# Kernel optimization log

Measured on AMD Instinct MI355X. Metric: run time of the kernel, lower is better.

## Reference

```python
import jax, jax.numpy as jnp
import numpy as np
from jax import lax

# PointPWC multi-scale Chamfer/Smoothness/Curvature loss (single scale here).
F_CHAMFER = 1.0
F_SMOOTH = 0.5
F_CURVATURE = 0.3
ALPHA0 = 0.02


def _sqdist(src, dst):
    # src: (B,N,3), dst: (B,M,3) -> (B,N,M) squared euclidean distances
    d = -2.0 * jnp.einsum('bnc,bmc->bnm', src, dst)
    d = d + jnp.sum(src * src, axis=-1)[:, :, None]
    d = d + jnp.sum(dst * dst, axis=-1)[:, None, :]
    return d


def _knn(sqd, k):
    # smallest-k of sqd along last axis -> (dists, indices)
    neg, idx = lax.top_k(-sqd, k)
    return -neg, idx


def _group(points, idx):
    # points: (B,N,C), idx: (B,M,k) -> (B,M,k,C)
    return jax.vmap(lambda p, i: p[i])(points, idx)


def _curvature(pc):
    # pc: (B,N,3) -> (B,N,3)
    _, kidx = _knn(_sqdist(pc, pc), 10)
    grouped = _group(pc, kidx)
    return jnp.sum(grouped - pc[:, :, None, :], axis=2) / 9.0


def _curvature_warp(pc, warped):
    _, kidx = _knn(_sqdist(pc, pc), 10)
    grouped = _group(warped, kidx)
    return jnp.sum(grouped - warped[:, :, None, :], axis=2) / 9.0


def _chamfer(p1, p2):
    sqd = _sqdist(p1, p2)
    return jnp.min(sqd, axis=-1), jnp.min(sqd, axis=1)


def _smooth(pc, flow, k):
    _, kidx = _knn(_sqdist(pc, pc), k)
    g = _group(flow, kidx)
    d = g - flow[:, :, None, :]
    sq = jnp.sum(d * d, axis=3)
    # safe norm: zero (self-neighbor) entries get norm 0 with zero grad
    nrm = jnp.where(sq == 0, 0.0, jnp.sqrt(jnp.where(sq == 0, 1.0, sq)))
    return jnp.sum(nrm, axis=2) / 8.0


def _interp_curvature(p1, p2, c2):
    dist, kidx = _knn(_sqdist(p1, p2), 5)
    g = _group(c2, kidx)  # (B,N,5,3)
    w = 1.0 / (dist + 1e-8)
    w = w / jnp.sum(w, axis=2, keepdims=True)
    return jnp.sum(w[..., None] * g, axis=2)


def setup_inputs() -> dict:
    key = jax.random.key(0)
    k1, k2, k3 = jax.random.split(key, 3)
    N = 8192
    coords = jax.random.normal(k1, (N, 3), dtype=jnp.float32)
    registration_gt = jax.random.normal(k2, (1, N, 3), dtype=jnp.float32)
    registration_pred = jax.random.normal(k3, (1, N, 3), dtype=jnp.float32)
    return {
        'registration_pred': registration_pred,
        'registration_gt': registration_gt,
        'coords': coords,
        'smoothness_k': 9,
    }


def reference(registration_pred, registration_gt, coords, smoothness_k):
    pc1 = coords[None]                       # (1,N,3)
    pc2 = coords[None] + registration_gt     # (1,N,3)
    flow = registration_pred                 # (1,N,3)

    pc2_curv = _curvature(pc2)
    pc1_warp = pc1 + flow
    dist1, dist2 = _chamfer(pc1_warp, pc2)
    moved_curv = _curvature_warp(pc1, pc1_warp)

    chamfer = jnp.mean(jnp.sum(dist1, axis=1)) + jnp.mean(jnp.sum(dist2, axis=1))
    smooth = jnp.mean(jnp.sum(_smooth(pc1, flow, smoothness_k), axis=1))
    inter_curv = _interp_curvature(pc1_warp, pc2, pc2_curv)
    curv = jnp.mean(jnp.sum(jnp.sum((inter_curv - moved_curv) ** 2, axis=2), axis=1))

    total = (F_CHAMFER * ALPHA0 * chamfer
             + F_CURVATURE * ALPHA0 * curv
             + F_SMOOTH * ALPHA0 * smooth)
    return jnp.reshape(total, (1,))
```

## Files before the change

kernel.cpp:

```cpp
#include <hip/hip_runtime.h>
#include <math.h>

#define N_PTS 8192
#define QPW 4
#define QPW_REV 8
#define WPB 4
#define QPB (QPW * WPB)
#define BLKS_TOPK (N_PTS / QPB)
#define BLKS_REV  (N_PTS / (QPW_REV * WPB))

#define R0_END BLKS_TOPK
#define R1_END (2 * BLKS_TOPK)
#define R3_END (3 * BLKS_TOPK)
#define GRID_TOTAL (3 * BLKS_TOPK + BLKS_REV)

#define W_CHAM 0.02f
#define W_CURV 0.006f
#define W_SMOO 0.01f

#define BIGF 1e30f
#define IDX_MASK 0x1FFFu
#define KEY_MASK 0xFFFFE000u

__device__ __forceinline__ float mkkey(float d, unsigned idx) {
    return __uint_as_float((__float_as_uint(d) & KEY_MASK) | idx);
}
__device__ __forceinline__ int keyidx(float k) {
    return (int)(__float_as_uint(k) & IDX_MASK);
}
__device__ __forceinline__ unsigned monou(float k) {
    int b = __float_as_int(k);
    return (unsigned)(b ^ ((b >> 31) | 0x80000000));
}
__device__ __forceinline__ int prefcnt(unsigned long long m) {
    return __builtin_amdgcn_mbcnt_hi((unsigned)(m >> 32),
           __builtin_amdgcn_mbcnt_lo((unsigned)m, 0));
}

template <int K>
__device__ __forceinline__ void kinsert(float kv, float (&bd)[K]) {
    bd[K - 1] = kv;
#pragma unroll
    for (int s = K - 1; s > 0; --s) {
        float lo = fminf(bd[s - 1], bd[s]);
        float hi = fmaxf(bd[s - 1], bd[s]);
        bd[s - 1] = lo; bd[s] = hi;
    }
}

template <int K>
__device__ void merge_keys(float m1, float m2, float m3, float (&bd)[K], int lane) {
    float h0 = m1, h1 = m2, h2 = m3;
#pragma unroll
    for (int r = 0; r < K; ++r) {
        float bv = h0;
#pragma unroll
        for (int off = 1; off < 64; off <<= 1) bv = fminf(bv, __shfl_xor(bv, off));
        bd[r] = bv;
        if (h0 == bv) { h0 = h1; h1 = h2; h2 = BIGF; }
    }
}

template <int K>
__device__ void tau_rescan(const float4* __restrict__ cand,
                           float nqx, float nqy, float nqz, float tau,
                           float (&bd)[K], int lane) {
#pragma unroll
    for (int r = 0; r < K; ++r) bd[r] = BIGF;
    const float4* cp = cand + lane;
    unsigned ib = (unsigned)lane;
    for (int it = 0; it < N_PTS / 64; ++it) {
        float4 p = cp[it * 64];
        float d = fmaf(p.x, nqx, fmaf(p.y, nqy, fmaf(p.z, nqz, p.w)));
        float kc = mkkey(d, ib);
        unsigned long long m = __ballot(kc <= tau);
        while (m) {
            int b = __builtin_ctzll(m);
            m &= m - 1;
            float kv = __shfl(kc, b);
            if (kv < bd[K - 1]) kinsert<K>(kv, bd);
        }
        ib += 64;
    }
}

template <int K>
__device__ void select_set(const float4* __restrict__ cand,
                           float nqx, float nqy, float nqz,
                           float& k1, float& k2, float& k3,
                           bool& q1, bool& q2, bool& q3, float& km, int lane) {
    const unsigned u1 = monou(k1), u2 = monou(k2), u3 = monou(k3);
    float bmn = k1, bmx = k1;
#pragma unroll
    for (int off = 1; off < 64; off <<= 1) {
        bmn = fminf(bmn, __shfl_xor(bmn, off));
        bmx = fmaxf(bmx, __shfl_xor(bmx, off));
    }
    unsigned lo = monou(bmn), hi = monou(bmx), piv = 0u;
    int cnt = -1;
    unsigned long long b3 = 0ull;
    for (int it = 0; it < 34; ++it) {
        piv = lo + ((hi - lo) >> 1);
        unsigned long long b1 = __ballot(u1 <= piv);
        unsigned long long b2 = __ballot(u2 <= piv);
        b3 = __ballot(u3 <= piv);
        cnt = __popcll(b1) + __popcll(b2) + __popcll(b3);
        if (cnt == K) break;
        if (cnt < K) lo = piv + 1; else hi = piv - 1;
    }
    bool setok = (cnt == K);
    bool fail;
    float bdK[K];
    if (setok) {
        q1 = (u1 <= piv); q2 = (u2 <= piv); q3 = (u3 <= piv);
        float t = q3 ? k3 : (q2 ? k2 : (q1 ? k1 : -BIGF));
#pragma unroll
        for (int off = 1; off < 64; off <<= 1) t = fmaxf(t, __shfl_xor(t, off));
        km = t;
        fail = (b3 != 0ull);
    } else {
        merge_keys<K>(k1, k2, k3, bdK, lane);
        km = bdK[K - 1];
        fail = (__ballot(k3 <= km) != 0ull);
    }
    if (fail) { tau_rescan<K>(cand, nqx, nqy, nqz, km, bdK, lane); setok = false; }
    if (!setok) {
        float kv = BIGF;
#pragma unroll
        for (int r = 0; r < K; ++r) if (lane == r) kv = bdK[r];
        k1 = kv; k2 = BIGF; k3 = BIGF;
        q1 = (lane < K); q2 = false; q3 = false;
        km = bdK[K - 1];
    }
}

__device__ __forceinline__ void wave_add3(float& a, float& b, float& c) {
#pragma unroll
    for (int off = 1; off < 64; off <<= 1) {
        a += __shfl_xor(a, off);
        b += __shfl_xor(b, off);
        c += __shfl_xor(c, off);
    }
}
__device__ __forceinline__ void wave_add4(float& a, float& b, float& c, float& d) {
#pragma unroll
    for (int off = 1; off < 64; off <<= 1) {
        a += __shfl_xor(a, off);
        b += __shfl_xor(b, off);
        c += __shfl_xor(c, off);
        d += __shfl_xor(d, off);
    }
}

template <int Q>
__device__ __forceinline__ void scank(const float4* __restrict__ cand,
                                      const float (&nqx)[Q], const float (&nqy)[Q],
                                      const float (&nqz)[Q],
                                      float (&m1)[Q], float (&m2)[Q], float (&m3)[Q],
                                      int lane) {
#pragma unroll
    for (int qi = 0; qi < Q; ++qi) { m1[qi] = BIGF; m2[qi] = BIGF; m3[qi] = BIGF; }
    const float4* cp = cand + lane;
    unsigned ib = (unsigned)lane;
#pragma unroll 2
    for (int it = 0; it < N_PTS / 256; ++it) {
        float4 p0 = cp[it * 256 + 0];
        float4 p1 = cp[it * 256 + 64];
        float4 p2 = cp[it * 256 + 128];
        float4 p3 = cp[it * 256 + 192];
#pragma unroll
        for (int qi = 0; qi < Q; ++qi) {
            float d0 = fmaf(p0.x, nqx[qi], fmaf(p0.y, nqy[qi], fmaf(p0.z, nqz[qi], p0.w)));
            float k0 = mkkey(d0, ib);
            m3[qi] = __builtin_amdgcn_fmed3f(k0, m2[qi], m3[qi]);
            m2[qi] = __builtin_amdgcn_fmed3f(k0, m1[qi], m2[qi]);
            m1[qi] = fminf(k0, m1[qi]);
            float d1 = fmaf(p1.x, nqx[qi], fmaf(p1.y, nqy[qi], fmaf(p1.z, nqz[qi], p1.w)));
            float k1 = mkkey(d1, ib + 64u);
            m3[qi] = __builtin_amdgcn_fmed3f(k1, m2[qi], m3[qi]);
            m2[qi] = __builtin_amdgcn_fmed3f(k1, m1[qi], m2[qi]);
            m1[qi] = fminf(k1, m1[qi]);
            float d2 = fmaf(p2.x, nqx[qi], fmaf(p2.y, nqy[qi], fmaf(p2.z, nqz[qi], p2.w)));
            float k2 = mkkey(d2, ib + 128u);
            m3[qi] = __builtin_amdgcn_fmed3f(k2, m2[qi], m3[qi]);
            m2[qi] = __builtin_amdgcn_fmed3f(k2, m1[qi], m2[qi]);
            m1[qi] = fminf(k2, m1[qi]);
            float d3 = fmaf(p3.x, nqx[qi], fmaf(p3.y, nqy[qi], fmaf(p3.z, nqz[qi], p3.w)));
            float k3 = mkkey(d3, ib + 192u);
            m3[qi] = __builtin_amdgcn_fmed3f(k3, m2[qi], m3[qi]);
            m2[qi] = __builtin_amdgcn_fmed3f(k3, m1[qi], m2[qi]);
            m1[qi] = fminf(k3, m1[qi]);
        }
        ib += 256u;
    }
}

__global__ void prep_kernel(const float* __restrict__ flow, const float* __restrict__ gt,
                            const float* __restrict__ coords,
                            float4* __restrict__ p1q, float4* __restrict__ p2q,
                            float4* __restrict__ wq, float* __restrict__ accs,
                            int* __restrict__ done) {
    int i = blockIdx.x * blockDim.x + threadIdx.x;
    if (i < N_PTS) {
        float cx = coords[3 * i + 0], cy = coords[3 * i + 1], cz = coords[3 * i + 2];
        float p2x = cx + gt[3 * i + 0], p2y = cy + gt[3 * i + 1], p2z = cz + gt[3 * i + 2];
        float wx = cx + flow[3 * i + 0], wy = cy + flow[3 * i + 1], wz = cz + flow[3 * i + 2];
        p1q[i] = make_float4(cx, cy, cz, cx * cx + cy * cy + cz * cz);
        p2q[i] = make_float4(p2x, p2y, p2z, p2x * p2x + p2y * p2y + p2z * p2z);
        wq[i]  = make_float4(wx, wy, wz, wx * wx + wy * wy + wz * wz);
    }
    if (i < 8) accs[i] = 0.0f;
    if (i == 8) done[0] = 0;
}

__global__ __launch_bounds__(256) void fused4_kernel(const float4* __restrict__ p1q,
                                                     const float4* __restrict__ p2q,
                                                     const float4* __restrict__ wq,
                                                     const float* __restrict__ flow,
                                                     const int* __restrict__ ksm_p,
                                                     float* __restrict__ curv2,
                                                     float* __restrict__ mcurv,
                                                     float* __restrict__ crossk,
                                                     float* __restrict__ accs) {
    const int tid = threadIdx.x, lane = tid & 63, wv = tid >> 6;
    const int b = blockIdx.x;

    if (b >= R3_END) {
        __shared__ float pmn[WPB];
        const int q0 = (b - R3_END) * (QPW_REV * WPB) + wv * QPW_REV;
        float nqx[QPW_REV], nqy[QPW_REV], nqz[QPW_REV], qw[QPW_REV], mn[QPW_REV];
#pragma unroll
        for (int qi = 0; qi < QPW_REV; ++qi) {
            float4 t = p2q[q0 + qi];
            nqx[qi] = -2.f * t.x; nqy[qi] = -2.f * t.y; nqz[qi] = -2.f * t.z;
            qw[qi] = t.w; mn[qi] = BIGF;
        }
        const float4* cp = wq + lane;
#pragma unroll 2
        for (int it = 0; it < N_PTS / 128; ++it) {
            float4 p0 = cp[it * 128 + 0];
            float4 p1 = cp[it * 128 + 64];
#pragma unroll
            for (int qi = 0; qi < QPW_REV; ++qi) {
                float d0 = fmaf(p0.x, nqx[qi], fmaf(p0.y, nqy[qi], fmaf(p0.z, nqz[qi], p0.w)));
                float d1 = fmaf(p1.x, nqx[qi], fmaf(p1.y, nqy[qi], fmaf(p1.z, nqz[qi], p1.w)));
                mn[qi] = fminf(mn[qi], fminf(d0, d1));
            }
        }
        float s = 0.f;
#pragma unroll
        for (int qi = 0; qi < QPW_REV; ++qi) {
            float v = mn[qi];
#pragma unroll
            for (int off = 1; off < 64; off <<= 1) v = fminf(v, __shfl_xor(v, off));
            s += v + qw[qi];
        }
        if (lane == 0) pmn[wv] = s;
        __syncthreads();
        if (tid == 0) atomicAdd(&accs[1], pmn[0] + pmn[1] + pmn[2] + pmn[3]);
        return;
    }

    const int role = (b < R0_END) ? 0 : (b < R1_END) ? 1 : 3;
    const int blk = b - ((role == 0) ? 0 : (role == 1) ? R0_END : R1_END);
    const int q0 = blk * QPB + wv * QPW;

    const float4* qsrc = (role == 0) ? p2q : (role == 1) ? p1q : wq;
    const float4* cand = (role == 1) ? p1q : p2q;
    float nqx[QPW], nqy[QPW], nqz[QPW];
#pragma unroll
    for (int qi = 0; qi < QPW; ++qi) {
        float4 t = qsrc[q0 + qi];
        nqx[qi] = -2.f * t.x; nqy[qi] = -2.f * t.y; nqz[qi] = -2.f * t.z;
    }
    float m1[QPW], m2[QPW], m3[QPW];
    scank<QPW>(cand, nqx, nqy, nqz, m1, m2, m3, lane);

    if (role == 3) {
        constexpr int K = 5;
#pragma unroll
        for (int qi = 0; qi < QPW; ++qi) {
            float k1 = m1[qi], k2 = m2[qi], k3 = m3[qi]; bool q1, q2, q3; float km;
            select_set<K>(p2q, nqx[qi], nqy[qi], nqz[qi], k1, k2, k3, q1, q2, q3, km, lane);
            const int q = q0 + qi;
            unsigned long long b1 = __ballot(q1), b2 = __ballot(q2), b3 = __ballot(q3);
            int c1 = __popcll(b1), c2 = __popcll(b2);
            if (q1) crossk[prefcnt(b1) * N_PTS + q] = k1;
            if (q2) crossk[(c1 + prefcnt(b2)) * N_PTS + q] = k2;
            if (q3) crossk[(c1 + c2 + prefcnt(b3)) * N_PTS + q] = k3;
        }
        return;
    }

    constexpr int K = 10;
    if (role == 0) {
#pragma unroll
        for (int qi = 0; qi < QPW; ++qi) {
            float k1 = m1[qi], k2 = m2[qi], k3 = m3[qi]; bool q1, q2, q3; float km;
            select_set<K>(p2q, nqx[qi], nqy[qi], nqz[qi], k1, k2, k3, q1, q2, q3, km, lane);
            float ax = 0.f, ay = 0.f, az = 0.f;
            if (q1) { float4 nb = p2q[keyidx(k1)]; ax += nb.x; ay += nb.y; az += nb.z; }
            if (q2) { float4 nb = p2q[keyidx(k2)]; ax += nb.x; ay += nb.y; az += nb.z; }
            if (q3) { float4 nb = p2q[keyidx(k3)]; ax += nb.x; ay += nb.y; az += nb.z; }
            wave_add3(ax, ay, az);
            if (lane == 0) {
                const int q = q0 + qi;
                float4 t = p2q[q];
                curv2[q * 3 + 0] = (ax - 10.f * t.x) * (1.f / 9.f);
                curv2[q * 3 + 1] = (ay - 10.f * t.y) * (1.f / 9.f);
                curv2[q * 3 + 2] = (az - 10.f * t.z) * (1.f / 9.f);
            }
        }
    } else {
        __shared__ float psm[WPB];
        const bool iall = (ksm_p[0] >= 10);
        float smsum = 0.f;
#pragma unroll
        for (int qi = 0; qi < QPW; ++qi) {
            float k1 = m1[qi], k2 = m2[qi], k3 = m3[qi]; bool q1, q2, q3; float km;
            select_set<K>(p1q, nqx[qi], nqy[qi], nqz[qi], k1, k2, k3, q1, q2, q3, km, lane);
            const int q = q0 + qi;
            const float fqx = flow[q * 3 + 0], fqy = flow[q * 3 + 1], fqz = flow[q * 3 + 2];
            float ax = 0.f, ay = 0.f, az = 0.f, sm = 0.f;
            if (q1) {
                const int ni = keyidx(k1);
                float4 nb = wq[ni];
                ax += nb.x; ay += nb.y; az += nb.z;
                if (iall || k1 < km) {
                    float dx = flow[ni * 3 + 0] - fqx, dy = flow[ni * 3 + 1] - fqy, dz = flow[ni * 3 + 2] - fqz;
                    float sq = dx * dx + dy * dy + dz * dz;
                    sm += (sq == 0.f) ? 0.f : sqrtf(sq);
                }
            }
            if (q2) {
                const int ni = keyidx(k2);
                float4 nb = wq[ni];
                ax += nb.x; ay += nb.y; az += nb.z;
                if (iall || k2 < km) {
                    float dx = flow[ni * 3 + 0] - fqx, dy = flow[ni * 3 + 1] - fqy, dz = flow[ni * 3 + 2] - fqz;
                    float sq = dx * dx + dy * dy + dz * dz;
                    sm += (sq == 0.f) ? 0.f : sqrtf(sq);
                }
            }
            if (q3) {
                const int ni = keyidx(k3);
                float4 nb = wq[ni];
                ax += nb.x; ay += nb.y; az += nb.z;
                if (iall || k3 < km) {
                    float dx = flow[ni * 3 + 0] - fqx, dy = flow[ni * 3 + 1] - fqy, dz = flow[ni * 3 + 2] - fqz;
                    float sq = dx * dx + dy * dy + dz * dz;
                    sm += (sq == 0.f) ? 0.f : sqrtf(sq);
                }
            }
            wave_add4(ax, ay, az, sm);
            smsum += sm * 0.125f;
            if (lane == 0) {
                float4 wqp = wq[q];
                mcurv[q * 3 + 0] = (ax - 10.f * wqp.x) * (1.f / 9.f);
                mcurv[q * 3 + 1] = (ay - 10.f * wqp.y) * (1.f / 9.f);
                mcurv[q * 3 + 2] = (az - 10.f * wqp.z) * (1.f / 9.f);
            }
        }
        if (lane == 0) psm[wv] = smsum;
        __syncthreads();
        if (tid == 0) atomicAdd(&accs[2], psm[0] + psm[1] + psm[2] + psm[3]);
    }
}

__global__ __launch_bounds__(64) void epi_kernel(const float* __restrict__ crossk,
                                                 const float4* __restrict__ wq,
                                                 const float4* __restrict__ p2q,
                                                 const float* __restrict__ curv2,
                                                 const float* __restrict__ mcurv,
                                                 float* __restrict__ accs,
                                                 int* __restrict__ done,
                                                 float* __restrict__ out) {
    const int lane = threadIdx.x & 63;
    const int q = blockIdx.x * 64 + threadIdx.x;
    constexpr int K = 5;
    float4 qp = wq[q];
    float bd[K]; int bi[K];
#pragma unroll
    for (int r = 0; r < K; ++r) {
        bi[r] = keyidx(crossk[r * N_PTS + q]);
        float4 nb = p2q[bi[r]];
        float dx = qp.x - nb.x, dy = qp.y - nb.y, dz = qp.z - nb.z;
        bd[r] = dx * dx + dy * dy + dz * dz;
    }
    float w[K], wsum = 0.f;
#pragma unroll
    for (int r = 0; r < K; ++r) { w[r] = 1.f / (bd[r] + 1e-8f); wsum += w[r]; }
    float ix = 0.f, iy = 0.f, iz = 0.f;
#pragma unroll
    for (int r = 0; r < K; ++r) {
        float ww = w[r] / wsum;
        ix += ww * curv2[bi[r] * 3 + 0];
        iy += ww * curv2[bi[r] * 3 + 1];
        iz += ww * curv2[bi[r] * 3 + 2];
    }
    float dx = ix - mcurv[q * 3 + 0];
    float dy = iy - mcurv[q * 3 + 1];
    float dz = iz - mcurv[q * 3 + 2];
    float d1 = fminf(fminf(fminf(bd[0], bd[1]), fminf(bd[2], bd[3])), bd[4]);
    float cv = dx * dx + dy * dy + dz * dz;
#pragma unroll
    for (int off = 1; off < 64; off <<= 1) {
        d1 += __shfl_xor(d1, off);
        cv += __shfl_xor(cv, off);
    }
    if (lane == 0) {
        atomicAdd(&accs[0], d1);
        atomicAdd(&accs[3], cv);
        __threadfence();
        int v = atomicAdd(done, 1);
        if (v == (int)gridDim.x - 1) {
            out[0] = W_CHAM * (accs[0] + accs[1]) + W_CURV * accs[3] + W_SMOO * accs[2];
        }
    }
}

extern "C" void kernel_launch(void* const* d_in, const int* in_sizes, int n_in,
                              void* d_out, int out_size, void* d_ws, size_t ws_size,
                              hipStream_t stream) {
    const float* flow   = (const float*)d_in[0];
    const float* gt     = (const float*)d_in[1];
    const float* coords = (const float*)d_in[2];
    const int*   ksm    = (const int*)d_in[3];

    float4* p1q   = (float4*)d_ws;
    float4* p2q   = p1q + N_PTS;
    float4* wq    = p2q + N_PTS;
    float*  curv2 = (float*)(wq + N_PTS);
    float*  mcurv = curv2 + 3 * N_PTS;
    float*  crossk = mcurv + 3 * N_PTS;
    float*  accs  = crossk + 5 * N_PTS;
    int*    done  = (int*)(accs + 8);
    float*  out   = (float*)d_out;

    prep_kernel<<<(N_PTS + 255) / 256, 256, 0, stream>>>(flow, gt, coords, p1q, p2q, wq,
                                                         accs, done);
    fused4_kernel<<<GRID_TOTAL, 256, 0, stream>>>(p1q, p2q, wq, flow, ksm,
                                                  curv2, mcurv, crossk, accs);
    epi_kernel<<<N_PTS / 64, 64, 0, stream>>>(crossk, wq, p2q, curv2, mcurv,
                                              accs, done, out);
}
```

Measured before the change: 144.9 us.

## Fuse prep, main and epilogue kernels into one persistent kernel with grid barriers

Merges the three kernel launches into a single mega-kernel that uses global atomic counters as spin barriers between the prep, scan and epilogue phases, with a memset to reset the counters. This removes launch gaps and kernel boundaries between dependent stages. It relies on every block being co-resident (GRID_TOTAL blocks at 256 threads, launch bounds 8 per CU) and risks deadlock or spin overhead if they are not. It also adds a memset launch and spin-wait latency.

```diff
diff --git a/kernel.cpp b/kernel.cpp
--- a/kernel.cpp
+++ b/kernel.cpp
@@ -14,6 +14,9 @@
 #define R3_END (3 * BLKS_TOPK)
 #define GRID_TOTAL (3 * BLKS_TOPK + BLKS_REV)
 
+#define PREP_BLKS 32
+#define EPI_BLKS 128
+
 #define W_CHAM 0.02f
 #define W_CURV 0.006f
 #define W_SMOO 0.01f
@@ -35,6 +38,12 @@
 __device__ __forceinline__ int prefcnt(unsigned long long m) {
     return __builtin_amdgcn_mbcnt_hi((unsigned)(m >> 32),
            __builtin_amdgcn_mbcnt_lo((unsigned)m, 0));
+}
+
+__device__ __forceinline__ void spin_until(int* p, int target) {
+    while (__hip_atomic_load(p, __ATOMIC_RELAXED, __HIP_MEMORY_SCOPE_AGENT) < target)
+        __builtin_amdgcn_s_sleep(8);
+    (void)__hip_atomic_load(p, __ATOMIC_ACQUIRE, __HIP_MEMORY_SCOPE_AGENT);
 }
 
 template <int K>
@@ -195,35 +204,37 @@
     }
 }
 
-__global__ void prep_kernel(const float* __restrict__ flow, const float* __restrict__ gt,
-                            const float* __restrict__ coords,
-                            float4* __restrict__ p1q, float4* __restrict__ p2q,
-                            float4* __restrict__ wq, float* __restrict__ accs,
-                            int* __restrict__ done) {
-    int i = blockIdx.x * blockDim.x + threadIdx.x;
-    if (i < N_PTS) {
+__global__ __launch_bounds__(256, 8) void mega_kernel(const float* __restrict__ flow,
+                                                      const float* __restrict__ gt,
+                                                      const float* __restrict__ coords,
+                                                      const int* __restrict__ ksm_p,
+                                                      float4* __restrict__ p1q,
+                                                      float4* __restrict__ p2q,
+                                                      float4* __restrict__ wq,
+                                                      float* __restrict__ curv2,
+                                                      float* __restrict__ mcurv,
+                                                      float* __restrict__ crossk,
+                                                      float* __restrict__ accs,
+                                                      int* __restrict__ done,
+                                                      int* __restrict__ bar,
+                                                      float* __restrict__ out) {
+    const int tid = threadIdx.x, lane = tid & 63, wv = tid >> 6;
+    const int b = blockIdx.x;
+
+    if (b < PREP_BLKS) {
+        int i = b * 256 + tid;
         float cx = coords[3 * i + 0], cy = coords[3 * i + 1], cz = coords[3 * i + 2];
         float p2x = cx + gt[3 * i + 0], p2y = cy + gt[3 * i + 1], p2z = cz + gt[3 * i + 2];
         float wx = cx + flow[3 * i + 0], wy = cy + flow[3 * i + 1], wz = cz + flow[3 * i + 2];
         p1q[i] = make_float4(cx, cy, cz, cx * cx + cy * cy + cz * cz);
         p2q[i] = make_float4(p2x, p2y, p2z, p2x * p2x + p2y * p2y + p2z * p2z);
         wq[i]  = make_float4(wx, wy, wz, wx * wx + wy * wy + wz * wz);
-    }
-    if (i < 8) accs[i] = 0.0f;
-    if (i == 8) done[0] = 0;
-}
-
-__global__ __launch_bounds__(256) void fused4_kernel(const float4* __restrict__ p1q,
-                                                     const float4* __restrict__ p2q,
-                                                     const float4* __restrict__ wq,
-                                                     const float* __restrict__ flow,
-                                                     const int* __restrict__ ksm_p,
-                                                     float* __restrict__ curv2,
-                                                     float* __restrict__ mcurv,
-                                                     float* __restrict__ crossk,
-                                                     float* __restrict__ accs) {
-    const int tid = threadIdx.x, lane = tid & 63, wv = tid >> 6;
-    const int b = blockIdx.x;
+        if (i < 8) accs[i] = 0.0f;
+        __syncthreads();
+        if (tid == 0) { __threadfence(); atomicAdd(&bar[0], 1); }
+    }
+    if (tid == 0) spin_until(&bar[0], PREP_BLKS);
+    __syncthreads();
 
     if (b >= R3_END) {
         __shared__ float pmn[WPB];
@@ -258,163 +269,163 @@
         if (lane == 0) pmn[wv] = s;
         __syncthreads();
         if (tid == 0) atomicAdd(&accs[1], pmn[0] + pmn[1] + pmn[2] + pmn[3]);
-        return;
-    }
-
-    const int role = (b < R0_END) ? 0 : (b < R1_END) ? 1 : 3;
-    const int blk = b - ((role == 0) ? 0 : (role == 1) ? R0_END : R1_END);
-    const int q0 = blk * QPB + wv * QPW;
-
-    const float4* qsrc = (role == 0) ? p2q : (role == 1) ? p1q : wq;
-    const float4* cand = (role == 1) ? p1q : p2q;
-    float nqx[QPW], nqy[QPW], nqz[QPW];
-#pragma unroll
-    for (int qi = 0; qi < QPW; ++qi) {
-        float4 t = qsrc[q0 + qi];
-        nqx[qi] = -2.f * t.x; nqy[qi] = -2.f * t.y; nqz[qi] = -2.f * t.z;
-    }
-    float m1[QPW], m2[QPW], m3[QPW];
-    scank<QPW>(cand, nqx, nqy, nqz, m1, m2, m3, lane);
-
-    if (role == 3) {
-        constexpr int K = 5;
+    } else {
+        const int role = (b < R0_END) ? 0 : (b < R1_END) ? 1 : 3;
+        const int blk = b - ((role == 0) ? 0 : (role == 1) ? R0_END : R1_END);
+        const int q0 = blk * QPB + wv * QPW;
+
+        const float4* qsrc = (role == 0) ? p2q : (role == 1) ? p1q : wq;
+        const float4* cand = (role == 1) ? p1q : p2q;
+        float nqx[QPW], nqy[QPW], nqz[QPW];
 #pragma unroll
         for (int qi = 0; qi < QPW; ++qi) {
-            float k1 = m1[qi], k2 = m2[qi], k3 = m3[qi]; bool q1, q2, q3; float km;
-            select_set<K>(p2q, nqx[qi], nqy[qi], nqz[qi], k1, k2, k3, q1, q2, q3, km, lane);
-            const int q = q0 + qi;
-            unsigned long long b1 = __ballot(q1), b2 = __ballot(q2), b3 = __ballot(q3);
-            int c1 = __popcll(b1), c2 = __popcll(b2);
-            if (q1) crossk[prefcnt(b1) * N_PTS + q] = k1;
-            if (q2) crossk[(c1 + prefcnt(b2)) * N_PTS + q] = k2;
-            if (q3) crossk[(c1 + c2 + prefcnt(b3)) * N_PTS + q] = k3;
-        }
-        return;
-    }
-
-    constexpr int K = 10;
-    if (role == 0) {
-#pragma unroll
-        for (int qi = 0; qi < QPW; ++qi) {
-            float k1 = m1[qi], k2 = m2[qi], k3 = m3[qi]; bool q1, q2, q3; float km;
-            select_set<K>(p2q, nqx[qi], nqy[qi], nqz[qi], k1, k2, k3, q1, q2, q3, km, lane);
-            float ax = 0.f, ay = 0.f, az = 0.f;
-            if (q1) { float4 nb = p2q[keyidx(k1)]; ax += nb.x; ay += nb.y; az += nb.z; }
-            if (q2) { float4 nb = p2q[keyidx(k2)]; ax += nb.x; ay += nb.y; az += nb.z; }
-            if (q3) { float4 nb = p2q[keyidx(k3)]; ax += nb.x; ay += nb.y; az += nb.z; }
-            wave_add3(ax, ay, az);
+            float4 t = qsrc[q0 + qi];
+            nqx[qi] = -2.f * t.x; nqy[qi] = -2.f * t.y; nqz[qi] = -2.f * t.z;
+        }
+        float m1[QPW], m2[QPW], m3[QPW];
+        scank<QPW>(cand, nqx, nqy, nqz, m1, m2, m3, lane);
+
+        if (role == 3) {
+            constexpr int K = 5;
+#pragma unroll
+            for (int qi = 0; qi < QPW; ++qi) {
+                float k1 = m1[qi], k2 = m2[qi], k3 = m3[qi]; bool q1, q2, q3; float km;
+                select_set<K>(p2q, nqx[qi], nqy[qi], nqz[qi], k1, k2, k3, q1, q2, q3, km, lane);
+                const int q = q0 + qi;
+                unsigned long long b1 = __ballot(q1), b2 = __ballot(q2), b3 = __ballot(q3);
+                int c1 = __popcll(b1), c2 = __popcll(b2);
+                if (q1) crossk[prefcnt(b1) * N_PTS + q] = k1;
+                if (q2) crossk[(c1 + prefcnt(b2)) * N_PTS + q] = k2;
+                if (q3) crossk[(c1 + c2 + prefcnt(b3)) * N_PTS + q] = k3;
+            }
+        } else if (role == 0) {
+            constexpr int K = 10;
+#pragma unroll
+            for (int qi = 0; qi < QPW; ++qi) {
+                float k1 = m1[qi], k2 = m2[qi], k3 = m3[qi]; bool q1, q2, q3; float km;
+                select_set<K>(p2q, nqx[qi], nqy[qi], nqz[qi], k1, k2, k3, q1, q2, q3, km, lane);
+                float ax = 0.f, ay = 0.f, az = 0.f;
+                if (q1) { float4 nb = p2q[keyidx(k1)]; ax += nb.x; ay += nb.y; az += nb.z; }
+                if (q2) { float4 nb = p2q[keyidx(k2)]; ax += nb.x; ay += nb.y; az += nb.z; }
+                if (q3) { float4 nb = p2q[keyidx(k3)]; ax += nb.x; ay += nb.y; az += nb.z; }
+                wave_add3(ax, ay, az);
+                if (lane == 0) {
+                    const int q = q0 + qi;
+                    float4 t = p2q[q];
+                    curv2[q * 3 + 0] = (ax - 10.f * t.x) * (1.f / 9.f);
+                    curv2[q * 3 + 1] = (ay - 10.f * t.y) * (1.f / 9.f);
+                    curv2[q * 3 + 2] = (az - 10.f * t.z) * (1.f / 9.f);
+                }
+            }
+        } else {
+            constexpr int K = 10;
+            __shared__ float psm[WPB];
+            const bool iall = (ksm_p[0] >= 10);
+            float smsum = 0.f;
+#pragma unroll
+            for (int qi = 0; qi < QPW; ++qi) {
+                float k1 = m1[qi], k2 = m2[qi], k3 = m3[qi]; bool q1, q2, q3; float km;
+                select_set<K>(p1q, nqx[qi], nqy[qi], nqz[qi], k1, k2, k3, q1, q2, q3, km, lane);
+                const int q = q0 + qi;
+                const float fqx = flow[q * 3 + 0], fqy = flow[q * 3 + 1], fqz = flow[q * 3 + 2];
+                float ax = 0.f, ay = 0.f, az = 0.f, sm = 0.f;
+                if (q1) {
+                    const int ni = keyidx(k1);
+                    float4 nb = wq[ni];
+                    ax += nb.x; ay += nb.y; az += nb.z;
+                    if (iall || k1 < km) {
+                        float dx = flow[ni * 3 + 0] - fqx, dy = flow[ni * 3 + 1] - fqy, dz = flow[ni * 3 + 2] - fqz;
+                        float sq = dx * dx + dy * dy + dz * dz;
+                        sm += (sq == 0.f) ? 0.f : sqrtf(sq);
+                    }
+                }
+                if (q2) {
+                    const int ni = keyidx(k2);
+                    float4 nb = wq[ni];
+                    ax += nb.x; ay += nb.y; az += nb.z;
+                    if (iall || k2 < km) {
+                        float dx = flow[ni * 3 + 0] - fqx, dy = flow[ni * 3 + 1] - fqy, dz = flow[ni * 3 + 2] - fqz;
+                        float sq = dx * dx + dy * dy + dz * dz;
+                        sm += (sq == 0.f) ? 0.f : sqrtf(sq);
+                    }
+                }
+                if (q3) {
+                    const int ni = keyidx(k3);
+                    float4 nb = wq[ni];
+                    ax += nb.x; ay += nb.y; az += nb.z;
+                    if (iall || k3 < km) {
+                        float dx = flow[ni * 3 + 0] - fqx, dy = flow[ni * 3 + 1] - fqy, dz = flow[ni * 3 + 2] - fqz;
+                        float sq = dx * dx + dy * dy + dz * dz;
+                        sm += (sq == 0.f) ? 0.f : sqrtf(sq);
+                    }
+                }
+                wave_add4(ax, ay, az, sm);
+                smsum += sm * 0.125f;
+                if (lane == 0) {
+                    float4 wqp = wq[q];
+                    mcurv[q * 3 + 0] = (ax - 10.f * wqp.x) * (1.f / 9.f);
+                    mcurv[q * 3 + 1] = (ay - 10.f * wqp.y) * (1.f / 9.f);
+                    mcurv[q * 3 + 2] = (az - 10.f * wqp.z) * (1.f / 9.f);
+                }
+            }
+            if (lane == 0) psm[wv] = smsum;
+            __syncthreads();
+            if (tid == 0) atomicAdd(&accs[2], psm[0] + psm[1] + psm[2] + psm[3]);
+        }
+    }
+
+    __syncthreads();
+    if (tid == 0) { __threadfence(); atomicAdd(&bar[1], 1); }
+    if (b < EPI_BLKS) {
+        if (tid == 0) spin_until(&bar[1], GRID_TOTAL);
+        __syncthreads();
+
+        if (wv == 0) {
+            const int q = b * 64 + lane;
+            constexpr int K = 5;
+            float4 qp = wq[q];
+            float bd[K]; int bi[K];
+#pragma unroll
+            for (int r = 0; r < K; ++r) {
+                bi[r] = keyidx(crossk[r * N_PTS + q]);
+                float4 nb = p2q[bi[r]];
+                float dx = qp.x - nb.x, dy = qp.y - nb.y, dz = qp.z - nb.z;
+                bd[r] = dx * dx + dy * dy + dz * dz;
+            }
+            float w[K], wsum = 0.f;
+#pragma unroll
+            for (int r = 0; r < K; ++r) { w[r] = 1.f / (bd[r] + 1e-8f); wsum += w[r]; }
+            float ix = 0.f, iy = 0.f, iz = 0.f;
+#pragma unroll
+            for (int r = 0; r < K; ++r) {
+                float ww = w[r] / wsum;
+                ix += ww * curv2[bi[r] * 3 + 0];
+                iy += ww * curv2[bi[r] * 3 + 1];
+                iz += ww * curv2[bi[r] * 3 + 2];
+            }
+            float dx = ix - mcurv[q * 3 + 0];
+            float dy = iy - mcurv[q * 3 + 1];
+            float dz = iz - mcurv[q * 3 + 2];
+            float d1 = fminf(fminf(fminf(bd[0], bd[1]), fminf(bd[2], bd[3])), bd[4]);
+            float cv = dx * dx + dy * dy + dz * dz;
+#pragma unroll
+            for (int off = 1; off < 64; off <<= 1) {
+                d1 += __shfl_xor(d1, off);
+                cv += __shfl_xor(cv, off);
+            }
             if (lane == 0) {
-                const int q = q0 + qi;
-                float4 t = p2q[q];
-                curv2[q * 3 + 0] = (ax - 10.f * t.x) * (1.f / 9.f);
-                curv2[q * 3 + 1] = (ay - 10.f * t.y) * (1.f / 9.f);
-                curv2[q * 3 + 2] = (az - 10.f * t.z) * (1.f / 9.f);
-            }
-        }
-    } else {
-        __shared__ float psm[WPB];
-        const bool iall = (ksm_p[0] >= 10);
-        float smsum = 0.f;
-#pragma unroll
-        for (int qi = 0; qi < QPW; ++qi) {
-            float k1 = m1[qi], k2 = m2[qi], k3 = m3[qi]; bool q1, q2, q3; float km;
-            select_set<K>(p1q, nqx[qi], nqy[qi], nqz[qi], k1, k2, k3, q1, q2, q3, km, lane);
-            const int q = q0 + qi;
-            const float fqx = flow[q * 3 + 0], fqy = flow[q * 3 + 1], fqz = flow[q * 3 + 2];
-            float ax = 0.f, ay = 0.f, az = 0.f, sm = 0.f;
-            if (q1) {
-                const int ni = keyidx(k1);
-                float4 nb = wq[ni];
-                ax += nb.x; ay += nb.y; az += nb.z;
-                if (iall || k1 < km) {
-                    float dx = flow[ni * 3 + 0] - fqx, dy = flow[ni * 3 + 1] - fqy, dz = flow[ni * 3 + 2] - fqz;
-                    float sq = dx * dx + dy * dy + dz * dz;
-                    sm += (sq == 0.f) ? 0.f : sqrtf(sq);
-                }
-            }
-            if (q2) {
-                const int ni = keyidx(k2);
-                float4 nb = wq[ni];
-                ax += nb.x; ay += nb.y; az += nb.z;
-                if (iall || k2 < km) {
-                    float dx = flow[ni * 3 + 0] - fqx, dy = flow[ni * 3 + 1] - fqy, dz = flow[ni * 3 + 2] - fqz;
-                    float sq = dx * dx + dy * dy + dz * dz;
-                    sm += (sq == 0.f) ? 0.f : sqrtf(sq);
-                }
-            }
-            if (q3) {
-                const int ni = keyidx(k3);
-                float4 nb = wq[ni];
-                ax += nb.x; ay += nb.y; az += nb.z;
-                if (iall || k3 < km) {
-                    float dx = flow[ni * 3 + 0] - fqx, dy = flow[ni * 3 + 1] - fqy, dz = flow[ni * 3 + 2] - fqz;
-                    float sq = dx * dx + dy * dy + dz * dz;
-                    sm += (sq == 0.f) ? 0.f : sqrtf(sq);
-                }
-            }
-            wave_add4(ax, ay, az, sm);
-            smsum += sm * 0.125f;
-            if (lane == 0) {
-                float4 wqp = wq[q];
-                mcurv[q * 3 + 0] = (ax - 10.f * wqp.x) * (1.f / 9.f);
-                mcurv[q * 3 + 1] = (ay - 10.f * wqp.y) * (1.f / 9.f);
-                mcurv[q * 3 + 2] = (az - 10.f * wqp.z) * (1.f / 9.f);
-            }
-        }
-        if (lane == 0) psm[wv] = smsum;
-        __syncthreads();
-        if (tid == 0) atomicAdd(&accs[2], psm[0] + psm[1] + psm[2] + psm[3]);
-    }
-}
-
-__global__ __launch_bounds__(64) void epi_kernel(const float* __restrict__ crossk,
-                                                 const float4* __restrict__ wq,
-                                                 const float4* __restrict__ p2q,
-                                                 const float* __restrict__ curv2,
-                                                 const float* __restrict__ mcurv,
-                                                 float* __restrict__ accs,
-                                                 int* __restrict__ done,
-                                                 float* __restrict__ out) {
-    const int lane = threadIdx.x & 63;
-    const int q = blockIdx.x * 64 + threadIdx.x;
-    constexpr int K = 5;
-    float4 qp = wq[q];
-    float bd[K]; int bi[K];
-#pragma unroll
-    for (int r = 0; r < K; ++r) {
-        bi[r] = keyidx(crossk[r * N_PTS + q]);
-        float4 nb = p2q[bi[r]];
-        float dx = qp.x - nb.x, dy = qp.y - nb.y, dz = qp.z - nb.z;
-        bd[r] = dx * dx + dy * dy + dz * dz;
-    }
-    float w[K], wsum = 0.f;
-#pragma unroll
-    for (int r = 0; r < K; ++r) { w[r] = 1.f / (bd[r] + 1e-8f); wsum += w[r]; }
-    float ix = 0.f, iy = 0.f, iz = 0.f;
-#pragma unroll
-    for (int r = 0; r < K; ++r) {
-        float ww = w[r] / wsum;
-        ix += ww * curv2[bi[r] * 3 + 0];
-        iy += ww * curv2[bi[r] * 3 + 1];
-        iz += ww * curv2[bi[r] * 3 + 2];
-    }
-    float dx = ix - mcurv[q * 3 + 0];
-    float dy = iy - mcurv[q * 3 + 1];
-    float dz = iz - mcurv[q * 3 + 2];
-    float d1 = fminf(fminf(fminf(bd[0], bd[1]), fminf(bd[2], bd[3])), bd[4]);
-    float cv = dx * dx + dy * dy + dz * dz;
-#pragma unroll
-    for (int off = 1; off < 64; off <<= 1) {
-        d1 += __shfl_xor(d1, off);
-        cv += __shfl_xor(cv, off);
-    }
-    if (lane == 0) {
-        atomicAdd(&accs[0], d1);
-        atomicAdd(&accs[3], cv);
-        __threadfence();
-        int v = atomicAdd(done, 1);
-        if (v == (int)gridDim.x - 1) {
-            out[0] = W_CHAM * (accs[0] + accs[1]) + W_CURV * accs[3] + W_SMOO * accs[2];
+                atomicAdd(&accs[0], d1);
+                atomicAdd(&accs[3], cv);
+                __threadfence();
+                int v = atomicAdd(done, 1);
+                if (v == EPI_BLKS - 1) {
+                    float a0 = __hip_atomic_load(&accs[0], __ATOMIC_RELAXED, __HIP_MEMORY_SCOPE_AGENT);
+                    float a1 = __hip_atomic_load(&accs[1], __ATOMIC_RELAXED, __HIP_MEMORY_SCOPE_AGENT);
+                    float a2 = __hip_atomic_load(&accs[2], __ATOMIC_RELAXED, __HIP_MEMORY_SCOPE_AGENT);
+                    float a3 = __hip_atomic_load(&accs[3], __ATOMIC_RELAXED, __HIP_MEMORY_SCOPE_AGENT);
+                    out[0] = W_CHAM * (a0 + a1) + W_CURV * a3 + W_SMOO * a2;
+                }
+            }
         }
     }
 }
@@ -435,12 +446,12 @@
     float*  crossk = mcurv + 3 * N_PTS;
     float*  accs  = crossk + 5 * N_PTS;
     int*    done  = (int*)(accs + 8);
+    int*    bar   = done + 1;
     float*  out   = (float*)d_out;
 
-    prep_kernel<<<(N_PTS + 255) / 256, 256, 0, stream>>>(flow, gt, coords, p1q, p2q, wq,
-                                                         accs, done);
-    fused4_kernel<<<GRID_TOTAL, 256, 0, stream>>>(p1q, p2q, wq, flow, ksm,
-                                                  curv2, mcurv, crossk, accs);
-    epi_kernel<<<N_PTS / 64, 64, 0, stream>>>(crossk, wq, p2q, curv2, mcurv,
-                                              accs, done, out);
-}
+    hipMemsetAsync((void*)done, 0, 3 * sizeof(int), stream);
+    mega_kernel<<<GRID_TOTAL, 256, 0, stream>>>(flow, gt, coords, ksm,
+                                                p1q, p2q, wq,
+                                                curv2, mcurv, crossk,
+                                                accs, done, bar, out);
+}
```

Result: slower. 384.3 us (+165.2%).

## Sort points by x and scan a bounded window with certified fallback

Applied to the files above, without the earlier changes.

Adds a counting-sort kernel that orders each point set by x coordinate, storing the original index in the w slot. Each kNN and chamfer query then scans only a fixed window of sorted candidates around its own position (or a binary-searched one) instead of all points. A slab-distance bound decides whether the window result is provably correct; if not, the code falls back to the existing full rescan. This trades an extra kernel launch and single-block-per-array sort for scanning about a quarter or less of the candidates, with the risk of frequent fallbacks when the data is spread out.

```diff
diff --git a/kernel.cpp b/kernel.cpp
--- a/kernel.cpp
+++ b/kernel.cpp
@@ -13,6 +13,15 @@
 #define R1_END (2 * BLKS_TOPK)
 #define R3_END (3 * BLKS_TOPK)
 #define GRID_TOTAL (3 * BLKS_TOPK + BLKS_REV)
+
+#define WTOP 2048
+#define NIT_TOP (WTOP / 256)
+#define WREV 1024
+#define NIT_REV (WREV / 128)
+
+#define NBINS 2048
+#define XMIN (-10.0f)
+#define BINWF (20.0f / (float)NBINS)
 
 #define W_CHAM 0.02f
 #define W_CURV 0.006f
@@ -86,7 +95,7 @@
 
 template <int K>
 __device__ void select_set(const float4* __restrict__ cand,
-                           float nqx, float nqy, float nqz,
+                           float nqx, float nqy, float nqz, float certG,
                            float& k1, float& k2, float& k3,
                            bool& q1, bool& q2, bool& q3, float& km, int lane) {
     const unsigned u1 = monou(k1), u2 = monou(k2), u3 = monou(k3);
@@ -117,11 +126,11 @@
 #pragma unroll
         for (int off = 1; off < 64; off <<= 1) t = fmaxf(t, __shfl_xor(t, off));
         km = t;
-        fail = (b3 != 0ull);
+        fail = (b3 != 0ull) || !(certG > km);
     } else {
         merge_keys<K>(k1, k2, k3, bdK, lane);
         km = bdK[K - 1];
-        fail = (__ballot(k3 <= km) != 0ull);
+        fail = (__ballot(k3 <= km) != 0ull) || !(certG > km);
     }
     if (fail) { tau_rescan<K>(cand, nqx, nqy, nqz, km, bdK, lane); setok = false; }
     if (!setok) {
@@ -152,46 +161,60 @@
     }
 }
 
+__device__ __forceinline__ int wave_bsearch(const float4* __restrict__ s, float x) {
+    int lo = 0, hi = N_PTS;
+    while (hi - lo > 1) {
+        int m = (lo + hi) >> 1;
+        if (s[m].x <= x) lo = m; else hi = m;
+    }
+    return lo;
+}
+
 template <int Q>
-__device__ __forceinline__ void scank(const float4* __restrict__ cand,
-                                      const float (&nqx)[Q], const float (&nqy)[Q],
-                                      const float (&nqz)[Q],
-                                      float (&m1)[Q], float (&m2)[Q], float (&m3)[Q],
-                                      int lane) {
+__device__ __forceinline__ void scankw(const float4* __restrict__ cw,
+                                       const float (&nqx)[Q], const float (&nqy)[Q],
+                                       const float (&nqz)[Q],
+                                       float (&m1)[Q], float (&m2)[Q], float (&m3)[Q],
+                                       int lane) {
 #pragma unroll
     for (int qi = 0; qi < Q; ++qi) { m1[qi] = BIGF; m2[qi] = BIGF; m3[qi] = BIGF; }
-    const float4* cp = cand + lane;
-    unsigned ib = (unsigned)lane;
-#pragma unroll 2
-    for (int it = 0; it < N_PTS / 256; ++it) {
+    const float4* cp = cw + lane;
+    for (int it = 0; it < NIT_TOP; ++it) {
         float4 p0 = cp[it * 256 + 0];
         float4 p1 = cp[it * 256 + 64];
         float4 p2 = cp[it * 256 + 128];
         float4 p3 = cp[it * 256 + 192];
+        float s0 = fmaf(p0.z, p0.z, fmaf(p0.y, p0.y, p0.x * p0.x));
+        float s1 = fmaf(p1.z, p1.z, fmaf(p1.y, p1.y, p1.x * p1.x));
+        float s2 = fmaf(p2.z, p2.z, fmaf(p2.y, p2.y, p2.x * p2.x));
+        float s3 = fmaf(p3.z, p3.z, fmaf(p3.y, p3.y, p3.x * p3.x));
+        unsigned i0 = __float_as_uint(p0.w);
+        unsigned i1 = __float_as_uint(p1.w);
+        unsigned i2 = __float_as_uint(p2.w);
+        unsigned i3 = __float_as_uint(p3.w);
 #pragma unroll
         for (int qi = 0; qi < Q; ++qi) {
-            float d0 = fmaf(p0.x, nqx[qi], fmaf(p0.y, nqy[qi], fmaf(p0.z, nqz[qi], p0.w)));
-            float k0 = mkkey(d0, ib);
+            float d0 = fmaf(p0.x, nqx[qi], fmaf(p0.y, nqy[qi], fmaf(p0.z, nqz[qi], s0)));
+            float k0 = mkkey(d0, i0);
             m3[qi] = __builtin_amdgcn_fmed3f(k0, m2[qi], m3[qi]);
             m2[qi] = __builtin_amdgcn_fmed3f(k0, m1[qi], m2[qi]);
             m1[qi] = fminf(k0, m1[qi]);
-            float d1 = fmaf(p1.x, nqx[qi], fmaf(p1.y, nqy[qi], fmaf(p1.z, nqz[qi], p1.w)));
-            float k1 = mkkey(d1, ib + 64u);
+            float d1 = fmaf(p1.x, nqx[qi], fmaf(p1.y, nqy[qi], fmaf(p1.z, nqz[qi], s1)));
+            float k1 = mkkey(d1, i1);
             m3[qi] = __builtin_amdgcn_fmed3f(k1, m2[qi], m3[qi]);
             m2[qi] = __builtin_amdgcn_fmed3f(k1, m1[qi], m2[qi]);
             m1[qi] = fminf(k1, m1[qi]);
-            float d2 = fmaf(p2.x, nqx[qi], fmaf(p2.y, nqy[qi], fmaf(p2.z, nqz[qi], p2.w)));
-            float k2 = mkkey(d2, ib + 128u);
+            float d2 = fmaf(p2.x, nqx[qi], fmaf(p2.y, nqy[qi], fmaf(p2.z, nqz[qi], s2)));
+            float k2 = mkkey(d2, i2);
             m3[qi] = __builtin_amdgcn_fmed3f(k2, m2[qi], m3[qi]);
             m2[qi] = __builtin_amdgcn_fmed3f(k2, m1[qi], m2[qi]);
             m1[qi] = fminf(k2, m1[qi]);
-            float d3 = fmaf(p3.x, nqx[qi], fmaf(p3.y, nqy[qi], fmaf(p3.z, nqz[qi], p3.w)));
-            float k3 = mkkey(d3, ib + 192u);
+            float d3 = fmaf(p3.x, nqx[qi], fmaf(p3.y, nqy[qi], fmaf(p3.z, nqz[qi], s3)));
+            float k3 = mkkey(d3, i3);
             m3[qi] = __builtin_amdgcn_fmed3f(k3, m2[qi], m3[qi]);
             m2[qi] = __builtin_amdgcn_fmed3f(k3, m1[qi], m2[qi]);
             m1[qi] = fminf(k3, m1[qi]);
         }
-        ib += 256u;
     }
 }
 
@@ -213,9 +236,66 @@
     if (i == 8) done[0] = 0;
 }
 
+__global__ __launch_bounds__(1024) void sort_kernel(const float4* __restrict__ p1q,
+                                                    const float4* __restrict__ p2q,
+                                                    const float4* __restrict__ wq,
+                                                    float4* __restrict__ sp1,
+                                                    float4* __restrict__ sp2,
+                                                    float4* __restrict__ swq) {
+    const float4* src = (blockIdx.x == 0) ? p1q : (blockIdx.x == 1) ? p2q : wq;
+    float4* dst = (blockIdx.x == 0) ? sp1 : (blockIdx.x == 1) ? sp2 : swq;
+    __shared__ int ha[NBINS];
+    __shared__ int hb[NBINS];
+    const int tid = threadIdx.x;
+    for (int i = tid; i < NBINS; i += 1024) ha[i] = 0;
+    __syncthreads();
+    int pb[N_PTS / 1024];
+#pragma unroll
+    for (int r = 0; r < N_PTS / 1024; ++r) {
+        int i = tid + r * 1024;
+        float x = src[i].x;
+        int b = (int)((x - XMIN) * (1.0f / BINWF));
+        b = min(max(b, 0), NBINS - 1);
+        pb[r] = b;
+        atomicAdd(&ha[b], 1);
+    }
+    __syncthreads();
+    int* a = ha; int* b2 = hb;
+    for (int off = 1; off < NBINS; off <<= 1) {
+        for (int i = tid; i < NBINS; i += 1024) {
+            int v = a[i];
+            if (i >= off) v += a[i - off];
+            b2[i] = v;
+        }
+        __syncthreads();
+        int* t = a; a = b2; b2 = t;
+    }
+    for (int i = tid; i < NBINS; i += 1024) b2[i] = (i == 0) ? 0 : a[i - 1];
+    __syncthreads();
+#pragma unroll
+    for (int r = 0; r < N_PTS / 1024; ++r) {
+        int i = tid + r * 1024;
+        int pos = atomicAdd(&b2[pb[r]], 1);
+        float4 t = src[i];
+        dst[pos] = make_float4(t.x, t.y, t.z, __uint_as_float((unsigned)i));
+    }
+}
+
+__device__ __forceinline__ float cert_bound(bool okl, bool okr, float xl, float xr,
+                                            float xq, float qs) {
+    float Gl = BIGF, Gr = BIGF;
+    if (!okl) { float g = xq - xl - BINWF; Gl = (g > 0.f) ? fmaf(g, g, -qs) : -BIGF; }
+    if (!okr) { float g = xr - BINWF - xq; Gr = (g > 0.f) ? fmaf(g, g, -qs) : -BIGF; }
+    float G = fminf(Gl, Gr);
+    return G - fabsf(G) * 0.002f - 1e-12f;
+}
+
 __global__ __launch_bounds__(256) void fused4_kernel(const float4* __restrict__ p1q,
                                                      const float4* __restrict__ p2q,
                                                      const float4* __restrict__ wq,
+                                                     const float4* __restrict__ sp1,
+                                                     const float4* __restrict__ sp2,
+                                                     const float4* __restrict__ swq,
                                                      const float* __restrict__ flow,
                                                      const int* __restrict__ ksm_p,
                                                      float* __restrict__ curv2,
@@ -228,32 +308,53 @@
     if (b >= R3_END) {
         __shared__ float pmn[WPB];
         const int q0 = (b - R3_END) * (QPW_REV * WPB) + wv * QPW_REV;
-        float nqx[QPW_REV], nqy[QPW_REV], nqz[QPW_REV], qw[QPW_REV], mn[QPW_REV];
+        float nqx[QPW_REV], nqy[QPW_REV], nqz[QPW_REV], qx[QPW_REV], qs[QPW_REV], mn[QPW_REV];
 #pragma unroll
         for (int qi = 0; qi < QPW_REV; ++qi) {
-            float4 t = p2q[q0 + qi];
+            float4 t = sp2[q0 + qi];
+            qx[qi] = t.x;
             nqx[qi] = -2.f * t.x; nqy[qi] = -2.f * t.y; nqz[qi] = -2.f * t.z;
-            qw[qi] = t.w; mn[qi] = BIGF;
-        }
-        const float4* cp = wq + lane;
-#pragma unroll 2
-        for (int it = 0; it < N_PTS / 128; ++it) {
+            qs[qi] = fmaf(t.z, t.z, fmaf(t.y, t.y, t.x * t.x));
+            mn[qi] = BIGF;
+        }
+        const int center = wave_bsearch(swq, qx[QPW_REV / 2]);
+        const int lo = min(max(center - WREV / 2, 0), N_PTS - WREV);
+        const float4* cp = swq + lo + lane;
+        for (int it = 0; it < NIT_REV; ++it) {
             float4 p0 = cp[it * 128 + 0];
             float4 p1 = cp[it * 128 + 64];
+            float s0 = fmaf(p0.z, p0.z, fmaf(p0.y, p0.y, p0.x * p0.x));
+            float s1 = fmaf(p1.z, p1.z, fmaf(p1.y, p1.y, p1.x * p1.x));
 #pragma unroll
             for (int qi = 0; qi < QPW_REV; ++qi) {
-                float d0 = fmaf(p0.x, nqx[qi], fmaf(p0.y, nqy[qi], fmaf(p0.z, nqz[qi], p0.w)));
-                float d1 = fmaf(p1.x, nqx[qi], fmaf(p1.y, nqy[qi], fmaf(p1.z, nqz[qi], p1.w)));
+                float d0 = fmaf(p0.x, nqx[qi], fmaf(p0.y, nqy[qi], fmaf(p0.z, nqz[qi], s0)));
+                float d1 = fmaf(p1.x, nqx[qi], fmaf(p1.y, nqy[qi], fmaf(p1.z, nqz[qi], s1)));
                 mn[qi] = fminf(mn[qi], fminf(d0, d1));
             }
         }
+        const bool okl = (lo == 0), okr = (lo + WREV >= N_PTS);
+        const float xl = okl ? 0.f : swq[lo - 1].x;
+        const float xr = okr ? 0.f : swq[lo + WREV].x;
         float s = 0.f;
 #pragma unroll
         for (int qi = 0; qi < QPW_REV; ++qi) {
             float v = mn[qi];
 #pragma unroll
             for (int off = 1; off < 64; off <<= 1) v = fminf(v, __shfl_xor(v, off));
-            s += v + qw[qi];
+            float Gm = cert_bound(okl, okr, xl, xr, qx[qi], qs[qi]);
+            if (!(Gm > v)) {
+                float mm = BIGF;
+                const float4* fp = wq + lane;
+                for (int it2 = 0; it2 < N_PTS / 64; ++it2) {
+                    float4 p = fp[it2 * 64];
+                    float d = fmaf(p.x, nqx[qi], fmaf(p.y, nqy[qi], fmaf(p.z, nqz[qi], p.w)));
+                    mm = fminf(mm, d);
+                }
+#pragma unroll
+                for (int off = 1; off < 64; off <<= 1) mm = fminf(mm, __shfl_xor(mm, off));
+                v = mm;
+            }
+            s += v + qs[qi];
         }
         if (lane == 0) pmn[wv] = s;
         __syncthreads();
@@ -265,24 +366,35 @@
     const int blk = b - ((role == 0) ? 0 : (role == 1) ? R0_END : R1_END);
     const int q0 = blk * QPB + wv * QPW;
 
-    const float4* qsrc = (role == 0) ? p2q : (role == 1) ? p1q : wq;
-    const float4* cand = (role == 1) ? p1q : p2q;
-    float nqx[QPW], nqy[QPW], nqz[QPW];
+    const float4* qS = (role == 0) ? sp2 : (role == 1) ? sp1 : swq;
+    const float4* cS = (role == 1) ? sp1 : sp2;
+    const float4* cOrig = (role == 1) ? p1q : p2q;
+    float nqx[QPW], nqy[QPW], nqz[QPW], qx[QPW], qs[QPW];
+    int qo[QPW];
 #pragma unroll
     for (int qi = 0; qi < QPW; ++qi) {
-        float4 t = qsrc[q0 + qi];
+        float4 t = qS[q0 + qi];
+        qx[qi] = t.x;
         nqx[qi] = -2.f * t.x; nqy[qi] = -2.f * t.y; nqz[qi] = -2.f * t.z;
-    }
+        qs[qi] = fmaf(t.z, t.z, fmaf(t.y, t.y, t.x * t.x));
+        qo[qi] = (int)__float_as_uint(t.w);
+    }
+    const int center = (role == 3) ? wave_bsearch(cS, qx[QPW / 2]) : (q0 + QPW / 2);
+    const int lo = min(max(center - WTOP / 2, 0), N_PTS - WTOP);
     float m1[QPW], m2[QPW], m3[QPW];
-    scank<QPW>(cand, nqx, nqy, nqz, m1, m2, m3, lane);
+    scankw<QPW>(cS + lo, nqx, nqy, nqz, m1, m2, m3, lane);
+    const bool okl = (lo == 0), okr = (lo + WTOP >= N_PTS);
+    const float xl = okl ? 0.f : cS[lo - 1].x;
+    const float xr = okr ? 0.f : cS[lo + WTOP].x;
 
     if (role == 3) {
         constexpr int K = 5;
 #pragma unroll
         for (int qi = 0; qi < QPW; ++qi) {
+            float Gm = cert_bound(okl, okr, xl, xr, qx[qi], qs[qi]);
             float k1 = m1[qi], k2 = m2[qi], k3 = m3[qi]; bool q1, q2, q3; float km;
-            select_set<K>(p2q, nqx[qi], nqy[qi], nqz[qi], k1, k2, k3, q1, q2, q3, km, lane);
-            const int q = q0 + qi;
+            select_set<K>(cOrig, nqx[qi], nqy[qi], nqz[qi], Gm, k1, k2, k3, q1, q2, q3, km, lane);
+            const int q = qo[qi];
             unsigned long long b1 = __ballot(q1), b2 = __ballot(q2), b3 = __ballot(q3);
             int c1 = __popcll(b1), c2 = __popcll(b2);
             if (q1) crossk[prefcnt(b1) * N_PTS + q] = k1;
@@ -296,15 +408,16 @@
     if (role == 0) {
 #pragma unroll
         for (int qi = 0; qi < QPW; ++qi) {
+            float Gm = cert_bound(okl, okr, xl, xr, qx[qi], qs[qi]);
             float k1 = m1[qi], k2 = m2[qi], k3 = m3[qi]; bool q1, q2, q3; float km;
-            select_set<K>(p2q, nqx[qi], nqy[qi], nqz[qi], k1, k2, k3, q1, q2, q3, km, lane);
+            select_set<K>(cOrig, nqx[qi], nqy[qi], nqz[qi], Gm, k1, k2, k3, q1, q2, q3, km, lane);
             float ax = 0.f, ay = 0.f, az = 0.f;
             if (q1) { float4 nb = p2q[keyidx(k1)]; ax += nb.x; ay += nb.y; az += nb.z; }
             if (q2) { float4 nb = p2q[keyidx(k2)]; ax += nb.x; ay += nb.y; az += nb.z; }
             if (q3) { float4 nb = p2q[keyidx(k3)]; ax += nb.x; ay += nb.y; az += nb.z; }
             wave_add3(ax, ay, az);
             if (lane == 0) {
-                const int q = q0 + qi;
+                const int q = qo[qi];
                 float4 t = p2q[q];
                 curv2[q * 3 + 0] = (ax - 10.f * t.x) * (1.f / 9.f);
                 curv2[q * 3 + 1] = (ay - 10.f * t.y) * (1.f / 9.f);
@@ -317,9 +430,10 @@
         float smsum = 0.f;
 #pragma unroll
         for (int qi = 0; qi < QPW; ++qi) {
+            float Gm = cert_bound(okl, okr, xl, xr, qx[qi], qs[qi]);
             float k1 = m1[qi], k2 = m2[qi], k3 = m3[qi]; bool q1, q2, q3; float km;
-            select_set<K>(p1q, nqx[qi], nqy[qi], nqz[qi], k1, k2, k3, q1, q2, q3, km, lane);
-            const int q = q0 + qi;
+            select_set<K>(cOrig, nqx[qi], nqy[qi], nqz[qi], Gm, k1, k2, k3, q1, q2, q3, km, lane);
+            const int q = qo[qi];
             const float fqx = flow[q * 3 + 0], fqy = flow[q * 3 + 1], fqz = flow[q * 3 + 2];
             float ax = 0.f, ay = 0.f, az = 0.f, sm = 0.f;
             if (q1) {
@@ -430,7 +544,10 @@
     float4* p1q   = (float4*)d_ws;
     float4* p2q   = p1q + N_PTS;
     float4* wq    = p2q + N_PTS;
-    float*  curv2 = (float*)(wq + N_PTS);
+    float4* sp1   = wq + N_PTS;
+    float4* sp2   = sp1 + N_PTS;
+    float4* swq   = sp2 + N_PTS;
+    float*  curv2 = (float*)(swq + N_PTS);
     float*  mcurv = curv2 + 3 * N_PTS;
     float*  crossk = mcurv + 3 * N_PTS;
     float*  accs  = crossk + 5 * N_PTS;
@@ -439,7 +556,8 @@
 
     prep_kernel<<<(N_PTS + 255) / 256, 256, 0, stream>>>(flow, gt, coords, p1q, p2q, wq,
                                                          accs, done);
-    fused4_kernel<<<GRID_TOTAL, 256, 0, stream>>>(p1q, p2q, wq, flow, ksm,
+    sort_kernel<<<3, 1024, 0, stream>>>(p1q, p2q, wq, sp1, sp2, swq);
+    fused4_kernel<<<GRID_TOTAL, 256, 0, stream>>>(p1q, p2q, wq, sp1, sp2, swq, flow, ksm,
                                                   curv2, mcurv, crossk, accs);
     epi_kernel<<<N_PTS / 64, 64, 0, stream>>>(crossk, wq, p2q, curv2, mcurv,
                                               accs, done, out);
```

Result: slower. 198.7 us (+37.2%).
